# Kernel tuning notes

Hardware: AMD Instinct MI355X
Metric: run time of the kernel (lower is better)

Reference implementation:

```python
import jax, jax.numpy as jnp
import numpy as np

N_NODES = 100000

def _mean_aggregate(h, edge_index, num_nodes):
    # PyG convention: edge_index[0]=source j, edge_index[1]=target i; mean over in-neighbors
    src, dst = edge_index[0], edge_index[1]
    summed = jax.ops.segment_sum(h[src], dst, num_segments=num_nodes)  # [N, D]
    cnt = jax.ops.segment_sum(jnp.ones((src.shape[0],), h.dtype), dst, num_segments=num_nodes)
    return summed / jnp.maximum(cnt, 1.0)[:, None]

def _sage_conv(h, edge_index, Wl, bl, Wr, num_nodes):
    agg = _mean_aggregate(h, edge_index, num_nodes)
    return agg @ Wl.T + bl + h @ Wr.T

def setup_inputs() -> dict:
    key = jax.random.key(0)
    ks = jax.random.split(key, 12)
    D = 64
    scale = 1.0 / np.sqrt(D)
    x = jax.random.normal(ks[0], (N_NODES, D), jnp.float32)
    edge_index = jax.random.randint(ks[1], (2, 1000000), 0, N_NODES, jnp.int32)
    edge_label_index = jax.random.randint(ks[2], (2, 200000), 0, N_NODES, jnp.int32)
    def w(k):
        return (jax.random.normal(k, (D, D), jnp.float32) * scale)
    return {
        'x': x,
        'edge_index': edge_index,
        'edge_label_index': edge_label_index,
        'W_lin': w(ks[3]), 'b_lin': jnp.zeros((D,), jnp.float32),
        'Wl1': w(ks[4]), 'bl1': jnp.zeros((D,), jnp.float32), 'Wr1': w(ks[5]),
        'Wl2': w(ks[6]), 'bl2': jnp.zeros((D,), jnp.float32), 'Wr2': w(ks[7]),
    }

def reference(x, edge_index, edge_label_index, W_lin, b_lin, Wl1, bl1, Wr1, Wl2, bl2, Wr2):
    h = x @ W_lin.T + b_lin                                   # node_lin
    h = jax.nn.relu(_sage_conv(h, edge_index, Wl1, bl1, Wr1, N_NODES))  # conv1 + relu
    h = _sage_conv(h, edge_index, Wl2, bl2, Wr2, N_NODES)               # conv2
    # edge dot-product classifier
    preds = jnp.sum(h[edge_label_index[0]] * h[edge_label_index[1]], axis=-1)  # [E_label]
    return preds
```

## Files before the change

kernel.cpp:

```cpp
#include <hip/hip_runtime.h>

#define DD 64
#define BW 256
#define NBMAX 512
#define CAPB 4096
#define CHUNK 8192
#define FILLPAD 16

typedef unsigned short u16;
typedef unsigned char u8;
typedef u16 ushort8v __attribute__((ext_vector_type(8)));
typedef short s16x8 __attribute__((ext_vector_type(8)));
typedef float f32x4 __attribute__((ext_vector_type(4)));
typedef float f32x2 __attribute__((ext_vector_type(2)));

__device__ __forceinline__ float bf2f(u16 u) {
    union { unsigned u32; float f; } x; x.u32 = (unsigned)u << 16; return x.f;
}
__device__ __forceinline__ u16 f2bf(float f) {
    union { float f; unsigned u; } x; x.f = f;
    unsigned r = (x.u + 0x7fffu + ((x.u >> 16) & 1u)) >> 16;
    return (u16)r;
}
__device__ __forceinline__ u8 f2fp8(float v) {
    return (u8)(__builtin_amdgcn_cvt_pk_fp8_f32(v, v, 0, false) & 0xff);
}

#define ACC16(u) do { \
    f32x2 _p; \
    _p = __builtin_amdgcn_cvt_pk_f32_fp8((int)(u).x, false); a[0]  += _p[0]; a[1]  += _p[1]; \
    _p = __builtin_amdgcn_cvt_pk_f32_fp8((int)(u).x, true);  a[2]  += _p[0]; a[3]  += _p[1]; \
    _p = __builtin_amdgcn_cvt_pk_f32_fp8((int)(u).y, false); a[4]  += _p[0]; a[5]  += _p[1]; \
    _p = __builtin_amdgcn_cvt_pk_f32_fp8((int)(u).y, true);  a[6]  += _p[0]; a[7]  += _p[1]; \
    _p = __builtin_amdgcn_cvt_pk_f32_fp8((int)(u).z, false); a[8]  += _p[0]; a[9]  += _p[1]; \
    _p = __builtin_amdgcn_cvt_pk_f32_fp8((int)(u).z, true);  a[10] += _p[0]; a[11] += _p[1]; \
    _p = __builtin_amdgcn_cvt_pk_f32_fp8((int)(u).w, false); a[12] += _p[0]; a[13] += _p[1]; \
    _p = __builtin_amdgcn_cvt_pk_f32_fp8((int)(u).w, true);  a[14] += _p[0]; a[15] += _p[1]; \
} while (0)

__global__ __launch_bounds__(256) void k_partlin(
    const int* __restrict__ ei, int n_edges, int nb_chunk,
    int* __restrict__ fill, unsigned* __restrict__ part,
    const float* __restrict__ w1, const float* __restrict__ w2,
    const float* __restrict__ w3, const float* __restrict__ w4,
    u16* __restrict__ wb,
    const float* __restrict__ A, const float* __restrict__ W,
    const float* __restrict__ bias, u16* __restrict__ out, u8* __restrict__ out8,
    int n_nodes) {
    int t = threadIdx.x;
    if ((int)blockIdx.x < nb_chunk) {
        __shared__ int hist[NBMAX];
        __shared__ int curs[NBMAX];
        {
            int i = blockIdx.x * 256 + t;
            if (i < 4 * DD * DD) {
                int mat = i >> 12, off = i & 4095;
                const float* src = (mat == 0) ? w1 : (mat == 1) ? w2 : (mat == 2) ? w3 : w4;
                wb[DD * DD + i] = f2bf(src[off]);
            }
        }
        hist[t] = 0; hist[256 + t] = 0;
        __syncthreads();
        int c0 = blockIdx.x * CHUNK;
        int c1 = min(n_edges, c0 + CHUNK);
        int nvec = (c1 - c0) & ~3;
        for (int e4 = c0 + t * 4; e4 < c0 + nvec; e4 += 1024) {
            int4 d4 = *(const int4*)(ei + n_edges + e4);
            atomicAdd(&hist[d4.x >> 8], 1);
            atomicAdd(&hist[d4.y >> 8], 1);
            atomicAdd(&hist[d4.z >> 8], 1);
            atomicAdd(&hist[d4.w >> 8], 1);
        }
        for (int e = c0 + nvec + t; e < c1; e += 256)
            atomicAdd(&hist[ei[n_edges + e] >> 8], 1);
        __syncthreads();
        #pragma unroll
        for (int k = 0; k < 2; ++k) {
            int idx = k * 256 + t;
            int h = hist[idx];
            int base = 0;
            if (h > 0) base = atomicAdd(&fill[idx * FILLPAD], h);
            curs[idx] = base;
        }
        __syncthreads();
        for (int e4 = c0 + t * 4; e4 < c0 + nvec; e4 += 1024) {
            int4 d4 = *(const int4*)(ei + n_edges + e4);
            int4 s4 = *(const int4*)(ei + e4);
            {
                int b = d4.x >> 8; int pos = atomicAdd(&curs[b], 1);
                if (pos < CAPB) part[(size_t)b * CAPB + pos] = ((unsigned)s4.x << 8) | (unsigned)(d4.x & 255);
            }
            {
                int b = d4.y >> 8; int pos = atomicAdd(&curs[b], 1);
                if (pos < CAPB) part[(size_t)b * CAPB + pos] = ((unsigned)s4.y << 8) | (unsigned)(d4.y & 255);
            }
            {
                int b = d4.z >> 8; int pos = atomicAdd(&curs[b], 1);
                if (pos < CAPB) part[(size_t)b * CAPB + pos] = ((unsigned)s4.z << 8) | (unsigned)(d4.z & 255);
            }
            {
                int b = d4.w >> 8; int pos = atomicAdd(&curs[b], 1);
                if (pos < CAPB) part[(size_t)b * CAPB + pos] = ((unsigned)s4.w << 8) | (unsigned)(d4.w & 255);
            }
        }
        for (int e = c0 + nvec + t; e < c1; e += 256) {
            int dst = ei[n_edges + e];
            int src = ei[e];
            int b = dst >> 8;
            int pos = atomicAdd(&curs[b], 1);
            if (pos < CAPB)
                part[(size_t)b * CAPB + pos] = ((unsigned)src << 8) | (unsigned)(dst & 255);
        }
    } else {
        int bid = (int)blockIdx.x - nb_chunk;
        int lane = t & 63;
        int col = lane & 15;
        int quad = lane >> 4;
        int m0 = bid * 64 + (t >> 6) * 16;
        int arow = m0 + col;
        if (arow > n_nodes - 1) arow = n_nodes - 1;

        f32x4 acc[4];
        #pragma unroll
        for (int nt = 0; nt < 4; ++nt) {
            float bv = bias[nt * 16 + col];
            acc[nt] = (f32x4){bv, bv, bv, bv};
        }
        #pragma unroll
        for (int ks = 0; ks < 2; ++ks) {
            int k0 = ks * 32 + quad * 8;
            const float* p = A + (size_t)arow * DD + k0;
            float4 v0 = *(const float4*)p;
            float4 v1 = *(const float4*)(p + 4);
            s16x8 a;
            a[0] = (short)f2bf(v0.x); a[1] = (short)f2bf(v0.y);
            a[2] = (short)f2bf(v0.z); a[3] = (short)f2bf(v0.w);
            a[4] = (short)f2bf(v1.x); a[5] = (short)f2bf(v1.y);
            a[6] = (short)f2bf(v1.z); a[7] = (short)f2bf(v1.w);
            #pragma unroll
            for (int nt = 0; nt < 4; ++nt) {
                const float* wp = W + (size_t)(nt * 16 + col) * DD + k0;
                float4 b0 = *(const float4*)wp;
                float4 b1 = *(const float4*)(wp + 4);
                s16x8 bfr;
                bfr[0] = (short)f2bf(b0.x); bfr[1] = (short)f2bf(b0.y);
                bfr[2] = (short)f2bf(b0.z); bfr[3] = (short)f2bf(b0.w);
                bfr[4] = (short)f2bf(b1.x); bfr[5] = (short)f2bf(b1.y);
                bfr[6] = (short)f2bf(b1.z); bfr[7] = (short)f2bf(b1.w);
                acc[nt] = __builtin_amdgcn_mfma_f32_16x16x32_bf16(a, bfr, acc[nt], 0, 0, 0);
            }
        }
        int mbase = m0 + quad * 4;
        #pragma unroll
        for (int nt = 0; nt < 4; ++nt)
            #pragma unroll
            for (int i = 0; i < 4; ++i) {
                int m = mbase + i;
                if (m < n_nodes) {
                    float v = acc[nt][i];
                    out[(size_t)m * DD + nt * 16 + col] = f2bf(v);
                    out8[(size_t)m * DD + nt * 16 + col] = f2fp8(v);
                }
            }
    }
}

__global__ __launch_bounds__(256) void k_build(const unsigned* __restrict__ part,
                        const int* __restrict__ fill,
                        int* __restrict__ row_start, int* __restrict__ row_deg,
                        int* __restrict__ csr, int n_nodes) {
    __shared__ int cnt_l[BW];
    __shared__ int sc[BW];
    __shared__ unsigned csr_l[CAPB];
    int t = threadIdx.x;
    int b = blockIdx.x;
    int beg = b * CAPB;
    int size = min(fill[b * FILLPAD], CAPB);

    cnt_l[t] = 0;
    __syncthreads();
    for (int j = t; j < size; j += 256)
        atomicAdd(&cnt_l[part[beg + j] & 255], 1);
    __syncthreads();
    int v0 = cnt_l[t];
    sc[t] = v0;
    cnt_l[t] = 0;
    __syncthreads();
    for (int off = 1; off < 256; off <<= 1) {
        int a = (t >= off) ? sc[t - off] : 0;
        __syncthreads();
        if (t >= off) sc[t] += a;
        __syncthreads();
    }
    {
        int n0 = b * BW + t;
        if (n0 < n_nodes) {
            row_start[n0] = beg + ((t == 0) ? 0 : sc[t - 1]);
            row_deg[n0] = v0;
        }
    }
    for (int j = t; j < size; j += 256) {
        unsigned p = part[beg + j];
        int dl = (int)(p & 255u);
        int pos = ((dl == 0) ? 0 : sc[dl - 1]) + atomicAdd(&cnt_l[dl], 1);
        csr_l[pos] = p >> 8;
    }
    __syncthreads();
    for (int i = t; i < size; i += 256) csr[beg + i] = (int)csr_l[i];
}

__global__ __launch_bounds__(256) void k_conv(
    const u16* __restrict__ h, const u8* __restrict__ h8,
    const int* __restrict__ row_start, const int* __restrict__ row_deg,
    const int* __restrict__ csr,
    const u16* __restrict__ Wl, const u16* __restrict__ Wr,
    const float* __restrict__ bias, u16* __restrict__ out, u8* __restrict__ out8,
    int n_nodes, int relu) {
    __shared__ u16 mean_l[64 * DD];
    int t = threadIdx.x;
    int w = t >> 6, lane = t & 63;
    int nn = lane >> 2;
    int r = lane & 3;
    int m0 = blockIdx.x * 64;

    {
        int li = w * 16 + nn;
        int n = m0 + li;
        int beg = 0, end = 0;
        if (n < n_nodes) { beg = row_start[n]; end = beg + row_deg[n]; }
        float a[16];
        #pragma unroll
        for (int kk = 0; kk < 16; ++kk) a[kk] = 0.f;
        int j = beg;
        for (; j + 3 < end; j += 4) {
            int s0 = csr[j], s1 = csr[j + 1], s2 = csr[j + 2], s3 = csr[j + 3];
            uint4 u0 = *(const uint4*)(h8 + (size_t)s0 * DD + r * 16);
            uint4 u1 = *(const uint4*)(h8 + (size_t)s1 * DD + r * 16);
            uint4 u2 = *(const uint4*)(h8 + (size_t)s2 * DD + r * 16);
            uint4 u3 = *(const uint4*)(h8 + (size_t)s3 * DD + r * 16);
            ACC16(u0); ACC16(u1); ACC16(u2); ACC16(u3);
        }
        for (; j < end; ++j) {
            uint4 u0 = *(const uint4*)(h8 + (size_t)csr[j] * DD + r * 16);
            ACC16(u0);
        }
        int deg = end - beg;
        float inv = (deg > 0) ? 1.0f / (float)deg : 0.0f;
        ushort8v o0, o1;
        #pragma unroll
        for (int kk = 0; kk < 8; ++kk) { o0[kk] = f2bf(a[kk] * inv); o1[kk] = f2bf(a[8 + kk] * inv); }
        *(ushort8v*)(mean_l + li * DD + r * 16) = o0;
        *(ushort8v*)(mean_l + li * DD + r * 16 + 8) = o1;
    }
    __threadfence_block();

    int col = lane & 15;
    int quad = lane >> 4;
    int arow = m0 + w * 16 + col;
    if (arow > n_nodes - 1) arow = n_nodes - 1;

    f32x4 acc[4];
    #pragma unroll
    for (int nt = 0; nt < 4; ++nt) {
        float bv = bias[nt * 16 + col];
        acc[nt] = (f32x4){bv, bv, bv, bv};
    }
    #pragma unroll
    for (int ks = 0; ks < 2; ++ks) {
        int k0 = ks * 32 + quad * 8;
        s16x8 am = *(const s16x8*)(mean_l + (w * 16 + col) * DD + k0);
        s16x8 ah = *(const s16x8*)(h + (size_t)arow * DD + k0);
        #pragma unroll
        for (int nt = 0; nt < 4; ++nt) {
            s16x8 bl = *(const s16x8*)(Wl + (nt * 16 + col) * DD + k0);
            acc[nt] = __builtin_amdgcn_mfma_f32_16x16x32_bf16(am, bl, acc[nt], 0, 0, 0);
            s16x8 br = *(const s16x8*)(Wr + (nt * 16 + col) * DD + k0);
            acc[nt] = __builtin_amdgcn_mfma_f32_16x16x32_bf16(ah, br, acc[nt], 0, 0, 0);
        }
    }
    int mbase = m0 + w * 16 + quad * 4;
    #pragma unroll
    for (int nt = 0; nt < 4; ++nt)
        #pragma unroll
        for (int i = 0; i < 4; ++i) {
            int m = mbase + i;
            if (m < n_nodes) {
                float v = acc[nt][i];
                if (relu) v = fmaxf(v, 0.f);
                out[(size_t)m * DD + nt * 16 + col] = f2bf(v);
                if (out8) out8[(size_t)m * DD + nt * 16 + col] = f2fp8(v);
            }
        }
}

__global__ void k_pred(const u16* __restrict__ h, const int* __restrict__ eli,
                       int n_label, float* __restrict__ out) {
    int t = threadIdx.x;
    int e = blockIdx.x * 16 + (t >> 4);
    if (e >= n_label) return;
    int g = (t >> 3) & 1;
    int r = t & 7;
    int node = g ? eli[n_label + e] : eli[e];
    ushort8v v = *(const ushort8v*)(h + (size_t)node * DD + r * 8);
    float s = 0.f;
    #pragma unroll
    for (int kk = 0; kk < 8; ++kk) {
        float f = bf2f(v[kk]);
        s += f * __shfl_xor(f, 8, 64);
    }
    #pragma unroll
    for (int off = 1; off < 8; off <<= 1) s += __shfl_xor(s, off, 64);
    if ((t & 15) == 0) out[e] = s;
}

extern "C" void kernel_launch(void* const* d_in, const int* in_sizes, int n_in,
                              void* d_out, int out_size, void* d_ws, size_t ws_size,
                              hipStream_t stream) {
    const float* x     = (const float*)d_in[0];
    const int*   ei    = (const int*)d_in[1];
    const int*   eli   = (const int*)d_in[2];
    const float* W_lin = (const float*)d_in[3];
    const float* b_lin = (const float*)d_in[4];
    const float* Wl1   = (const float*)d_in[5];
    const float* bl1   = (const float*)d_in[6];
    const float* Wr1   = (const float*)d_in[7];
    const float* Wl2   = (const float*)d_in[8];
    const float* bl2   = (const float*)d_in[9];
    const float* Wr2   = (const float*)d_in[10];

    int n_nodes = in_sizes[0] / DD;
    int n_edges = in_sizes[1] / 2;
    int n_label = in_sizes[2] / 2;
    float* out = (float*)d_out;

    int nb = (n_nodes + BW - 1) / BW;

    char* ws = (char*)d_ws;
    size_t hbytes = (size_t)n_nodes * DD * sizeof(u16);
    u16* hA   = (u16*)ws; ws += hbytes;
    u16* hB   = (u16*)ws; ws += hbytes;
    u8* h8A   = (u8*)ws;  ws += (size_t)n_nodes * DD;
    u8* h8B   = (u8*)ws;  ws += (size_t)n_nodes * DD;
    int* row_start = (int*)ws; ws += (size_t)((n_nodes + 3) & ~3) * sizeof(int);
    int* row_deg   = (int*)ws; ws += (size_t)((n_nodes + 3) & ~3) * sizeof(int);
    int* fill      = (int*)ws; ws += (size_t)NBMAX * FILLPAD * sizeof(int);
    u16* wb        = (u16*)ws; ws += 5 * DD * DD * sizeof(u16);
    unsigned* part = (unsigned*)ws; ws += (size_t)nb * CAPB * sizeof(unsigned);
    int* csr       = (int*)ws; ws += (size_t)nb * CAPB * sizeof(int);

    int nb_chunk = (n_edges + CHUNK - 1) / CHUNK;
    int nb_gemm = (n_nodes + 63) / 64;
    int nb_pred = (n_label + 15) / 16;

    (void)hipMemsetAsync(fill, 0, (size_t)NBMAX * FILLPAD * sizeof(int), stream);
    k_partlin<<<nb_chunk + nb_gemm, 256, 0, stream>>>(
        ei, n_edges, nb_chunk, fill, part,
        Wl1, Wr1, Wl2, Wr2, wb,
        x, W_lin, b_lin, hA, h8A, n_nodes);

    k_build<<<nb, 256, 0, stream>>>(part, fill, row_start, row_deg, csr, n_nodes);

    k_conv<<<nb_gemm, 256, 0, stream>>>(hA, h8A, row_start, row_deg, csr,
                                        wb + 4096, wb + 2 * 4096, bl1, hB, h8B, n_nodes, 1);

    k_conv<<<nb_gemm, 256, 0, stream>>>(hB, h8B, row_start, row_deg, csr,
                                        wb + 3 * 4096, wb + 4 * 4096, bl2, hA, nullptr, n_nodes, 0);

    k_pred<<<nb_pred, 256, 0, stream>>>(hA, eli, n_label, out);
}
```

Baseline: 199.0 us.

## Stage partitioned edge records in shared memory before coalesced global scatter

The edge-partition blocks now compute an exclusive prefix scan of the per-bucket histogram, scatter records into a shared-memory buffer grouped by bucket, then write them to global memory in order, using a binary search to recover each record's bucket. This turns scattered 4-byte global writes into mostly contiguous runs per bucket, which should cut write transactions. The cost is extra shared memory (a 32KB record buffer plus scan arrays, declared for every block including the GEMM blocks, which can lower occupancy), a scan with many barriers, and a 9-step binary search per record. It also adds an alignment guard on the vectorized loads.

```diff
diff --git a/kernel.cpp b/kernel.cpp
--- a/kernel.cpp
+++ b/kernel.cpp
@@ -47,10 +47,14 @@
     const float* __restrict__ A, const float* __restrict__ W,
     const float* __restrict__ bias, u16* __restrict__ out, u8* __restrict__ out8,
     int n_nodes) {
+    __shared__ unsigned rec[CHUNK];
+    __shared__ int hist[NBMAX];
+    __shared__ int sc[NBMAX];
+    __shared__ int scn[NBMAX + 1];
+    __shared__ int gbase[NBMAX];
+    __shared__ int curs[NBMAX];
     int t = threadIdx.x;
     if ((int)blockIdx.x < nb_chunk) {
-        __shared__ int hist[NBMAX];
-        __shared__ int curs[NBMAX];
         {
             int i = blockIdx.x * 256 + t;
             if (i < 4 * DD * DD) {
@@ -63,53 +67,80 @@
         __syncthreads();
         int c0 = blockIdx.x * CHUNK;
         int c1 = min(n_edges, c0 + CHUNK);
-        int nvec = (c1 - c0) & ~3;
-        for (int e4 = c0 + t * 4; e4 < c0 + nvec; e4 += 1024) {
-            int4 d4 = *(const int4*)(ei + n_edges + e4);
+        int nloc = c1 - c0;
+        int nvec = ((n_edges & 3) == 0) ? (nloc & ~3) : 0;
+        for (int e4 = t * 4; e4 < nvec; e4 += 1024) {
+            int4 d4 = *(const int4*)(ei + n_edges + c0 + e4);
             atomicAdd(&hist[d4.x >> 8], 1);
             atomicAdd(&hist[d4.y >> 8], 1);
             atomicAdd(&hist[d4.z >> 8], 1);
             atomicAdd(&hist[d4.w >> 8], 1);
         }
-        for (int e = c0 + nvec + t; e < c1; e += 256)
-            atomicAdd(&hist[ei[n_edges + e] >> 8], 1);
-        __syncthreads();
-        #pragma unroll
-        for (int k = 0; k < 2; ++k) {
-            int idx = k * 256 + t;
-            int h = hist[idx];
-            int base = 0;
-            if (h > 0) base = atomicAdd(&fill[idx * FILLPAD], h);
-            curs[idx] = base;
-        }
-        __syncthreads();
-        for (int e4 = c0 + t * 4; e4 < c0 + nvec; e4 += 1024) {
-            int4 d4 = *(const int4*)(ei + n_edges + e4);
-            int4 s4 = *(const int4*)(ei + e4);
+        for (int e = nvec + t; e < nloc; e += 256)
+            atomicAdd(&hist[ei[n_edges + c0 + e] >> 8], 1);
+        __syncthreads();
+        sc[t] = hist[t]; sc[256 + t] = hist[256 + t];
+        __syncthreads();
+        for (int off = 1; off < 256; off <<= 1) {
+            int a = (t >= off) ? sc[t - off] : 0;
+            int c = (t >= off) ? sc[256 + t - off] : 0;
+            __syncthreads();
+            if (t >= off) { sc[t] += a; sc[256 + t] += c; }
+            __syncthreads();
+        }
+        int tot0 = sc[255];
+        sc[256 + t] += tot0;
+        __syncthreads();
+        if (t == 0) scn[0] = 0;
+        scn[t + 1] = sc[t];
+        scn[257 + t] = sc[256 + t];
+        {
+            int h0 = hist[t];
+            gbase[t] = (h0 > 0) ? atomicAdd(&fill[t * FILLPAD], h0) : 0;
+            int h1 = hist[256 + t];
+            gbase[256 + t] = (h1 > 0) ? atomicAdd(&fill[(256 + t) * FILLPAD], h1) : 0;
+        }
+        curs[t] = 0; curs[256 + t] = 0;
+        __syncthreads();
+        for (int e4 = t * 4; e4 < nvec; e4 += 1024) {
+            int4 d4 = *(const int4*)(ei + n_edges + c0 + e4);
+            int4 s4 = *(const int4*)(ei + c0 + e4);
             {
-                int b = d4.x >> 8; int pos = atomicAdd(&curs[b], 1);
-                if (pos < CAPB) part[(size_t)b * CAPB + pos] = ((unsigned)s4.x << 8) | (unsigned)(d4.x & 255);
+                int b = d4.x >> 8; int p = scn[b] + atomicAdd(&curs[b], 1);
+                rec[p] = ((unsigned)s4.x << 8) | (unsigned)(d4.x & 255);
             }
             {
-                int b = d4.y >> 8; int pos = atomicAdd(&curs[b], 1);
-                if (pos < CAPB) part[(size_t)b * CAPB + pos] = ((unsigned)s4.y << 8) | (unsigned)(d4.y & 255);
+                int b = d4.y >> 8; int p = scn[b] + atomicAdd(&curs[b], 1);
+                rec[p] = ((unsigned)s4.y << 8) | (unsigned)(d4.y & 255);
             }
             {
-                int b = d4.z >> 8; int pos = atomicAdd(&curs[b], 1);
-                if (pos < CAPB) part[(size_t)b * CAPB + pos] = ((unsigned)s4.z << 8) | (unsigned)(d4.z & 255);
+                int b = d4.z >> 8; int p = scn[b] + atomicAdd(&curs[b], 1);
+                rec[p] = ((unsigned)s4.z << 8) | (unsigned)(d4.z & 255);
             }
             {
-                int b = d4.w >> 8; int pos = atomicAdd(&curs[b], 1);
-                if (pos < CAPB) part[(size_t)b * CAPB + pos] = ((unsigned)s4.w << 8) | (unsigned)(d4.w & 255);
-            }
-        }
-        for (int e = c0 + nvec + t; e < c1; e += 256) {
-            int dst = ei[n_edges + e];
-            int src = ei[e];
+                int b = d4.w >> 8; int p = scn[b] + atomicAdd(&curs[b], 1);
+                rec[p] = ((unsigned)s4.w << 8) | (unsigned)(d4.w & 255);
+            }
+        }
+        for (int e = nvec + t; e < nloc; e += 256) {
+            int dst = ei[n_edges + c0 + e];
+            int src = ei[c0 + e];
             int b = dst >> 8;
-            int pos = atomicAdd(&curs[b], 1);
-            if (pos < CAPB)
-                part[(size_t)b * CAPB + pos] = ((unsigned)src << 8) | (unsigned)(dst & 255);
+            int p = scn[b] + atomicAdd(&curs[b], 1);
+            rec[p] = ((unsigned)src << 8) | (unsigned)(dst & 255);
+        }
+        __syncthreads();
+        for (int i = t; i < nloc; i += 256) {
+            unsigned u = rec[i];
+            int lo = 0, hi = NBMAX;
+            #pragma unroll
+            for (int s = 0; s < 9; ++s) {
+                int mid = (lo + hi) >> 1;
+                if (scn[mid] <= i) lo = mid; else hi = mid;
+            }
+            int b = lo;
+            int pos = gbase[b] + (i - scn[b]);
+            if (pos < CAPB) part[(size_t)b * CAPB + pos] = u;
         }
     } else {
         int bid = (int)blockIdx.x - nb_chunk;
```

After: 207.8 us. 4.4% more time.
